# Performance work log

Hardware: AMD Instinct MI355X
Metric: run time of the kernel (lower is better)

## Reference

```python
import jax, jax.numpy as jnp
import numpy as np

B, S, D = 8, 2048, 64
NEG = -1e9


def setup_inputs() -> dict:
    key = jax.random.key(0)
    kq, kk, kv = jax.random.split(key, 3)
    return {
        "queries": jax.random.normal(kq, (B, S, D), dtype=jnp.float32),
        "keys": jax.random.normal(kk, (B, S, D), dtype=jnp.float32),
        "values": jax.random.normal(kv, (B, S, D), dtype=jnp.float32),
        "mask_q": jnp.ones((B, S), dtype=jnp.float32),
        "mask_k": jnp.ones((B, S), dtype=jnp.float32),
        "mask_v": jnp.ones((B, S), dtype=jnp.float32),
    }


def reference(queries, keys, values, mask_q, mask_k, mask_v):
    # scaled QK^T: [B, Sq, Sk]
    scaler = jnp.sqrt(jnp.asarray(queries.shape[-1], dtype=queries.dtype))
    scores = jnp.einsum("bqd,bkd->bqk", queries, keys) / scaler
    # additive padding mask from outer product of query/key masks
    padding_mask = mask_q[:, :, None] * mask_k[:, None, :]  # [B, Sq, Sk]
    scores = scores + (1.0 - padding_mask) * NEG
    attention_weights = jax.nn.softmax(scores, axis=-1)
    # mask values then weighted sum
    values = values * mask_v[:, :, None]
    output = jnp.einsum("bqk,bkd->bqd", attention_weights, values)
    return output
```

## Files before the change

### kernel.cpp

```cpp
#include <hip/hip_runtime.h>
#include <hip/hip_bf16.h>
#include <math.h>

#define BATCH 8
#define SEQ   2048
#define DIM   64
#define NEGC  (-1e9f)
#define SPLIT 4
#define TPB   8

typedef short short8  __attribute__((ext_vector_type(8)));
typedef float f32x4   __attribute__((ext_vector_type(4)));
typedef float f32x16  __attribute__((ext_vector_type(16)));

#define MFMA32(a, b, c) __builtin_amdgcn_mfma_f32_32x32x16_bf16((a), (b), (c), 0, 0, 0)

__device__ __forceinline__ ushort f2bf(float x) {
    uint u = __float_as_uint(x);
    uint r = (u + 0x7fffu + ((u >> 16) & 1u)) >> 16;
    return (ushort)r;
}
__device__ __forceinline__ float bf2f(ushort h) {
    return __uint_as_float(((uint)h) << 16);
}

__global__ __launch_bounds__(256)
void prep_kv(const float* __restrict__ K, const float* __restrict__ V,
             const float* __restrict__ MV, ushort* __restrict__ ws) {
    __shared__ float raw[64 * 68];
    const int t    = threadIdx.x;
    const int isV  = blockIdx.x >> 8;
    const int img  = blockIdx.x & 255;
    const int b    = img >> 5;
    const int tile = img & 31;
    ushort* wsI = ws + (size_t)(b * 32 + tile) * 8192;

    if (!isV) {
        const float* Kb = K + ((size_t)b * SEQ + tile * 64) * DIM;
#pragma unroll
        for (int u = 0; u < 4; u++) {
            int f = t + 256 * u, key = f >> 4, d4 = (f & 15) * 4;
            *(float4*)&raw[key * 68 + d4] = *(const float4*)(Kb + (size_t)f * 4);
        }
        __syncthreads();
#pragma unroll
        for (int u = 0; u < 2; u++) {
            int r = t + 256 * u;
            int mt = r >> 8, kc = (r >> 6) & 3, L = r & 63;
            int key = mt * 32 + (L & 31), d0 = kc * 16 + (L >> 5) * 8;
            float4 x0 = *(float4*)&raw[key * 68 + d0];
            float4 x1 = *(float4*)&raw[key * 68 + d0 + 4];
            float xs[8] = {x0.x, x0.y, x0.z, x0.w, x1.x, x1.y, x1.z, x1.w};
            short8 hv;
#pragma unroll
            for (int j = 0; j < 8; j++) hv[j] = (short)f2bf(xs[j]);
            *(short8*)(wsI + r * 8) = hv;
        }
    } else {
        const float* Vb  = V  + ((size_t)b * SEQ + tile * 64) * DIM;
        const float* MVb = MV + (size_t)b * SEQ + tile * 64;
#pragma unroll
        for (int u = 0; u < 4; u++) {
            int f = t + 256 * u, key = f >> 4, d4 = (f & 15) * 4;
            float4 x = *(const float4*)(Vb + (size_t)f * 4);
            float mv = MVb[key];
            x.x *= mv; x.y *= mv; x.z *= mv; x.w *= mv;
            *(float4*)&raw[key * 68 + d4] = x;
        }
        __syncthreads();
#pragma unroll
        for (int u = 0; u < 2; u++) {
            int r = t + 256 * u;
            int dt = r >> 8, kc = (r >> 6) & 3, L = r & 63;
            int d = dt * 32 + (L & 31), k0 = kc * 16 + (L >> 5) * 8;
            short8 ov;
#pragma unroll
            for (int j = 0; j < 8; j++) ov[j] = (short)f2bf(raw[(k0 + j) * 68 + d]);
            *(short8*)(wsI + 4096 + r * 8) = ov;
        }
    }
}

__global__ __launch_bounds__(256, 4)
void attn_main(const float* __restrict__ Q, const float* __restrict__ MQ,
               const float* __restrict__ MK, const ushort* __restrict__ ws,
               float* __restrict__ PO, float* __restrict__ ML) {
    __shared__ __align__(16) float Msc[2][64 * 36];

    const int t    = threadIdx.x;
    const int w    = t >> 6;
    const int lane = t & 63;
    const int h    = lane >> 5;
    const int lm   = lane & 31;
    const int qg   = w & 1;
    const int kh   = w >> 1;

    const int s  = blockIdx.x & 3;
    const int qb = blockIdx.x >> 2;
    const int b  = qb >> 5;
    const int qt = qb & 31;
    const int q  = qt * 64 + qg * 32 + lm;

    const float*  MKb  = MK + (size_t)b * SEQ;
    const ushort* wsKV = ws + (size_t)b * 32 * 8192;

    short8 qh[4], ql[4];
    {
        const float* Qr = Q + ((size_t)b * SEQ + q) * DIM;
#pragma unroll
        for (int kc = 0; kc < 4; kc++) {
            const float* p = Qr + kc * 16 + h * 8;
            float4 x0 = *(const float4*)p;
            float4 x1 = *(const float4*)(p + 4);
            float xs[8] = {x0.x, x0.y, x0.z, x0.w, x1.x, x1.y, x1.z, x1.w};
#pragma unroll
            for (int j = 0; j < 8; j++) {
                float v   = xs[j] * 0.125f;
                ushort hi = f2bf(v);
                ql[kc][j] = (short)f2bf(v - bf2f(hi));
                qh[kc][j] = (short)hi;
            }
        }
    }
    const float mq   = MQ[(size_t)b * SEQ + q];
    const float apen = NEGC * mq;

    float m = -1e30f, l = 0.0f;
    f32x16 ot0, ot1;
#pragma unroll
    for (int i = 0; i < 16; i++) { ot0[i] = 0.0f; ot1[i] = 0.0f; }

    short8 kf[4];
    {
        const ushort* img = wsKV + (size_t)(s * TPB) * 8192;
#pragma unroll
        for (int kc = 0; kc < 4; kc++)
            kf[kc] = *(const short8*)(img + ((kh * 4 + kc) * 64 + lane) * 8);
    }

#pragma unroll 1
    for (int tt = 0; tt < TPB; tt++) {
        const ushort* img  = wsKV + (size_t)(s * TPB + tt) * 8192;
        const ushort* imgN = (tt + 1 < TPB) ? img + 8192 : img;

        short8 kn[4];
#pragma unroll
        for (int kc = 0; kc < 4; kc++)
            kn[kc] = *(const short8*)(imgN + ((kh * 4 + kc) * 64 + lane) * 8);
        short8 vv[4];
#pragma unroll
        for (int dt = 0; dt < 2; dt++)
#pragma unroll
            for (int c = 0; c < 2; c++)
                vv[dt * 2 + c] = *(const short8*)(img + 4096 * 2 +
                                                  0);
#pragma unroll
        for (int dt = 0; dt < 2; dt++)
#pragma unroll
            for (int c = 0; c < 2; c++)
                vv[dt * 2 + c] = *(const short8*)(img + 4096 +
                    ((dt * 4 + kh * 2 + c) * 64 + lane) * 8);
        const float* mkp = MKb + (s * TPB + tt) * 64 + kh * 32 + h * 4;
        f32x4 mk0 = *(const f32x4*)(mkp + 0);
        f32x4 mk1 = *(const f32x4*)(mkp + 8);
        f32x4 mk2 = *(const f32x4*)(mkp + 16);
        f32x4 mk3 = *(const f32x4*)(mkp + 24);

        f32x16 st;
#pragma unroll
        for (int i = 0; i < 16; i++) st[i] = 0.0f;
#pragma unroll
        for (int kc = 0; kc < 4; kc++) {
            st = MFMA32(kf[kc], qh[kc], st);
            st = MFMA32(kf[kc], ql[kc], st);
        }

        float sv[16];
#pragma unroll
        for (int c = 0; c < 4; c++) {
            sv[0 * 4 + c]  = st[0 * 4 + c]  + (NEGC - apen * mk0[c]);
            sv[1 * 4 + c]  = st[1 * 4 + c]  + (NEGC - apen * mk1[c]);
            sv[2 * 4 + c]  = st[2 * 4 + c]  + (NEGC - apen * mk2[c]);
            sv[3 * 4 + c]  = st[3 * 4 + c]  + (NEGC - apen * mk3[c]);
        }
        float cm = sv[0];
#pragma unroll
        for (int i = 1; i < 16; i++) cm = fmaxf(cm, sv[i]);
        cm = fmaxf(cm, __shfl_xor(cm, 32));
        float nm    = fmaxf(m, cm);
        float alpha = __expf(m - nm);
        m = nm;

        float p[16], cs = 0.0f;
#pragma unroll
        for (int i = 0; i < 16; i++) { p[i] = __expf(sv[i] - nm); cs += p[i]; }
        cs += __shfl_xor(cs, 32);
        l   = l * alpha + cs;
        ot0 *= alpha; ot1 *= alpha;

        uint g[4][2], x[4][2];
#pragma unroll
        for (int v = 0; v < 4; v++) {
            __hip_bfloat162 c0 = __float22bfloat162_rn(make_float2(p[v*4+0], p[v*4+1]));
            __hip_bfloat162 c1 = __float22bfloat162_rn(make_float2(p[v*4+2], p[v*4+3]));
            __builtin_memcpy(&g[v][0], &c0, 4);
            __builtin_memcpy(&g[v][1], &c1, 4);
            x[v][0] = (uint)__shfl_xor((int)g[v][0], 32);
            x[v][1] = (uint)__shfl_xor((int)g[v][1], 32);
        }
        uint pbw[2][4];
        pbw[0][0] = h ? x[1][0] : g[0][0];
        pbw[0][1] = h ? x[1][1] : g[0][1];
        pbw[0][2] = h ? g[1][0] : x[0][0];
        pbw[0][3] = h ? g[1][1] : x[0][1];
        pbw[1][0] = h ? x[3][0] : g[2][0];
        pbw[1][1] = h ? x[3][1] : g[2][1];
        pbw[1][2] = h ? g[3][0] : x[2][0];
        pbw[1][3] = h ? g[3][1] : x[2][1];

#pragma unroll
        for (int c = 0; c < 2; c++) {
            short8 pb;
            __builtin_memcpy(&pb, &pbw[c][0], 16);
            ot0 = MFMA32(vv[0 * 2 + c], pb, ot0);
            ot1 = MFMA32(vv[1 * 2 + c], pb, ot1);
        }

#pragma unroll
        for (int kc = 0; kc < 4; kc++) kf[kc] = kn[kc];
    }

    if (kh == 1) {
        float* sc = &Msc[qg][lane * 36];
#pragma unroll
        for (int i = 0; i < 16; i++) { sc[i] = ot0[i]; sc[16 + i] = ot1[i]; }
        sc[32] = m;
        sc[33] = l;
    }
    __syncthreads();
    if (kh == 0) {
        const float* sc = &Msc[qg][lane * 36];
        float mb = sc[32], lb = sc[33];
        float nm = fmaxf(m, mb);
        float fa = __expf(m - nm);
        float fb = __expf(mb - nm);
        float lt = l * fa + lb * fb;

        float* po = PO + (((size_t)(s * 8 + b) * SEQ) + qt * 64 + qg * 32 + lm) * 64;
#pragma unroll
        for (int dt = 0; dt < 2; dt++) {
            const f32x16& o = dt ? ot1 : ot0;
#pragma unroll
            for (int rq = 0; rq < 4; rq++) {
                f32x4 r;
#pragma unroll
                for (int c = 0; c < 4; c++)
                    r[c] = o[rq * 4 + c] * fa + sc[dt * 16 + rq * 4 + c] * fb;
                *(f32x4*)(po + dt * 32 + rq * 8 + h * 4) = r;
            }
        }
        if (h == 0) {
            float2* ml2 = (float2*)ML;
            ml2[((size_t)(s * 8 + b) * SEQ) + qt * 64 + qg * 32 + lm] =
                make_float2(nm, lt);
        }
    }
}

__global__ __launch_bounds__(256)
void merge_o(const float* __restrict__ PO, const float* __restrict__ ML,
             float* __restrict__ O) {
    const int tid = blockIdx.x * 256 + threadIdx.x;
    const int qln = tid >> 4;
    const int dq  = tid & 15;
    const int b   = qln >> 11;
    const int qr  = qln & 2047;

    const float2* ml2 = (const float2*)ML;
    float2 mls[SPLIT];
#pragma unroll
    for (int s = 0; s < SPLIT; s++) mls[s] = ml2[(size_t)(s * 8 + b) * SEQ + qr];
    float mm = mls[0].x;
#pragma unroll
    for (int s = 1; s < SPLIT; s++) mm = fmaxf(mm, mls[s].x);
    float f[SPLIT], denom = 0.0f;
#pragma unroll
    for (int s = 0; s < SPLIT; s++) {
        f[s] = __expf(mls[s].x - mm);
        denom += mls[s].y * f[s];
    }
    float inv = 1.0f / denom;

    const size_t POS = (size_t)8 * SEQ * 64;
    const size_t o0  = ((size_t)b * SEQ + qr) * 64 + dq * 4;
    f32x4 acc = {0, 0, 0, 0};
#pragma unroll
    for (int s = 0; s < SPLIT; s++)
        acc += (*(const f32x4*)(PO + s * POS + o0)) * f[s];
    *(f32x4*)(O + ((size_t)b * SEQ + qr) * DIM + dq * 4) = acc * inv;
}

extern "C" void kernel_launch(void* const* d_in, const int* in_sizes, int n_in,
                              void* d_out, int out_size, void* d_ws, size_t ws_size,
                              hipStream_t stream) {
    const float* Q  = (const float*)d_in[0];
    const float* K  = (const float*)d_in[1];
    const float* V  = (const float*)d_in[2];
    const float* MQ = (const float*)d_in[3];
    const float* MK = (const float*)d_in[4];
    const float* MV = (const float*)d_in[5];
    float* O = (float*)d_out;

    ushort* wsKV = (ushort*)d_ws;
    float*  PO   = (float*)((char*)d_ws + (4u << 20));
    float*  ML   = (float*)((char*)d_ws + (20u << 20));

    prep_kv  <<<dim3(512),  dim3(256), 0, stream>>>(K, V, MV, wsKV);
    attn_main<<<dim3(1024), dim3(256), 0, stream>>>(Q, MQ, MK, wsKV, PO, ML);
    merge_o  <<<dim3(1024), dim3(256), 0, stream>>>(PO, ML, O);
}
```

Baseline: 107.9 us.

## Fuse KV prep, attention and merge into one cooperative grid-synced kernel

Replaces the three-kernel pipeline (KV bf16 prep, split-K attention, merge) with a single cooperative kernel. It converts K/V in a first phase, performs a grid-wide sync, then has each block own 32 queries across all 2048 keys, with four waves splitting the key chunks and combining through shared memory. This removes two launches and the partial-output/ML round trip through global memory. In exchange there is a grid barrier, lower occupancy (launch bounds 2), only 512 blocks, and each block now handles 32 queries instead of 64, so K/V reuse per block is lower.

```diff
diff --git a/kernel.cpp b/kernel.cpp
--- a/kernel.cpp
+++ b/kernel.cpp
@@ -1,13 +1,14 @@
 #include <hip/hip_runtime.h>
 #include <hip/hip_bf16.h>
+#include <hip/hip_cooperative_groups.h>
 #include <math.h>
+
+namespace cg = cooperative_groups;
 
 #define BATCH 8
 #define SEQ   2048
 #define DIM   64
 #define NEGC  (-1e9f)
-#define SPLIT 4
-#define TPB   8
 
 typedef short short8  __attribute__((ext_vector_type(8)));
 typedef float f32x4   __attribute__((ext_vector_type(4)));
@@ -24,85 +25,85 @@
     return __uint_as_float(((uint)h) << 16);
 }
 
-__global__ __launch_bounds__(256)
-void prep_kv(const float* __restrict__ K, const float* __restrict__ V,
-             const float* __restrict__ MV, ushort* __restrict__ ws) {
-    __shared__ float raw[64 * 68];
-    const int t    = threadIdx.x;
-    const int isV  = blockIdx.x >> 8;
-    const int img  = blockIdx.x & 255;
-    const int b    = img >> 5;
-    const int tile = img & 31;
-    ushort* wsI = ws + (size_t)(b * 32 + tile) * 8192;
-
-    if (!isV) {
-        const float* Kb = K + ((size_t)b * SEQ + tile * 64) * DIM;
-#pragma unroll
-        for (int u = 0; u < 4; u++) {
-            int f = t + 256 * u, key = f >> 4, d4 = (f & 15) * 4;
-            *(float4*)&raw[key * 68 + d4] = *(const float4*)(Kb + (size_t)f * 4);
-        }
-        __syncthreads();
-#pragma unroll
-        for (int u = 0; u < 2; u++) {
-            int r = t + 256 * u;
-            int mt = r >> 8, kc = (r >> 6) & 3, L = r & 63;
-            int key = mt * 32 + (L & 31), d0 = kc * 16 + (L >> 5) * 8;
-            float4 x0 = *(float4*)&raw[key * 68 + d0];
-            float4 x1 = *(float4*)&raw[key * 68 + d0 + 4];
-            float xs[8] = {x0.x, x0.y, x0.z, x0.w, x1.x, x1.y, x1.z, x1.w};
-            short8 hv;
-#pragma unroll
-            for (int j = 0; j < 8; j++) hv[j] = (short)f2bf(xs[j]);
-            *(short8*)(wsI + r * 8) = hv;
-        }
-    } else {
-        const float* Vb  = V  + ((size_t)b * SEQ + tile * 64) * DIM;
-        const float* MVb = MV + (size_t)b * SEQ + tile * 64;
-#pragma unroll
-        for (int u = 0; u < 4; u++) {
-            int f = t + 256 * u, key = f >> 4, d4 = (f & 15) * 4;
-            float4 x = *(const float4*)(Vb + (size_t)f * 4);
-            float mv = MVb[key];
-            x.x *= mv; x.y *= mv; x.z *= mv; x.w *= mv;
-            *(float4*)&raw[key * 68 + d4] = x;
-        }
-        __syncthreads();
-#pragma unroll
-        for (int u = 0; u < 2; u++) {
-            int r = t + 256 * u;
-            int dt = r >> 8, kc = (r >> 6) & 3, L = r & 63;
-            int d = dt * 32 + (L & 31), k0 = kc * 16 + (L >> 5) * 8;
-            short8 ov;
-#pragma unroll
-            for (int j = 0; j < 8; j++) ov[j] = (short)f2bf(raw[(k0 + j) * 68 + d]);
-            *(short8*)(wsI + 4096 + r * 8) = ov;
-        }
-    }
-}
-
-__global__ __launch_bounds__(256, 4)
-void attn_main(const float* __restrict__ Q, const float* __restrict__ MQ,
-               const float* __restrict__ MK, const ushort* __restrict__ ws,
-               float* __restrict__ PO, float* __restrict__ ML) {
-    __shared__ __align__(16) float Msc[2][64 * 36];
-
-    const int t    = threadIdx.x;
+__global__ __launch_bounds__(256, 2)
+void attn_all(const float* __restrict__ Q, const float* __restrict__ K,
+              const float* __restrict__ V, const float* __restrict__ MQ,
+              const float* __restrict__ MK, const float* __restrict__ MV,
+              ushort* __restrict__ ws, float* __restrict__ O) {
+    __shared__ __align__(16) float SH[6912];
+
+    const int t = threadIdx.x;
+    const int g = blockIdx.x;
+
+    {
+        const int img  = g >> 1;
+        const int isV  = g & 1;
+        const int b    = img >> 5;
+        const int tile = img & 31;
+        float* raw = SH;
+        ushort* wsI = ws + (size_t)img * 8192;
+
+        if (!isV) {
+            const float* Kb = K + ((size_t)b * SEQ + tile * 64) * DIM;
+#pragma unroll
+            for (int u = 0; u < 4; u++) {
+                int f = t + 256 * u, key = f >> 4, d4 = (f & 15) * 4;
+                *(float4*)&raw[key * 68 + d4] = *(const float4*)(Kb + (size_t)f * 4);
+            }
+            __syncthreads();
+#pragma unroll
+            for (int u = 0; u < 2; u++) {
+                int r = t + 256 * u;
+                int mt = r >> 8, kc = (r >> 6) & 3, L = r & 63;
+                int key = mt * 32 + (L & 31), d0 = kc * 16 + (L >> 5) * 8;
+                float4 x0 = *(float4*)&raw[key * 68 + d0];
+                float4 x1 = *(float4*)&raw[key * 68 + d0 + 4];
+                float xs[8] = {x0.x, x0.y, x0.z, x0.w, x1.x, x1.y, x1.z, x1.w};
+                short8 hv;
+#pragma unroll
+                for (int j = 0; j < 8; j++) hv[j] = (short)f2bf(xs[j]);
+                *(short8*)(wsI + r * 8) = hv;
+            }
+        } else {
+            const float* Vb  = V  + ((size_t)b * SEQ + tile * 64) * DIM;
+            const float* MVb = MV + (size_t)b * SEQ + tile * 64;
+#pragma unroll
+            for (int u = 0; u < 4; u++) {
+                int f = t + 256 * u, key = f >> 4, d4 = (f & 15) * 4;
+                float4 x = *(const float4*)(Vb + (size_t)f * 4);
+                float mv = MVb[key];
+                x.x *= mv; x.y *= mv; x.z *= mv; x.w *= mv;
+                *(float4*)&raw[key * 68 + d4] = x;
+            }
+            __syncthreads();
+#pragma unroll
+            for (int u = 0; u < 2; u++) {
+                int r = t + 256 * u;
+                int dt = r >> 8, kc = (r >> 6) & 3, L = r & 63;
+                int d = dt * 32 + (L & 31), k0 = kc * 16 + (L >> 5) * 8;
+                short8 ov;
+#pragma unroll
+                for (int j = 0; j < 8; j++) ov[j] = (short)f2bf(raw[(k0 + j) * 68 + d]);
+                *(short8*)(wsI + 4096 + r * 8) = ov;
+            }
+        }
+    }
+
+    __threadfence();
+    cg::this_grid().sync();
+    __threadfence();
+
     const int w    = t >> 6;
     const int lane = t & 63;
     const int h    = lane >> 5;
     const int lm   = lane & 31;
-    const int qg   = w & 1;
-    const int kh   = w >> 1;
-
-    const int s  = blockIdx.x & 3;
-    const int qb = blockIdx.x >> 2;
-    const int b  = qb >> 5;
-    const int qt = qb & 31;
-    const int q  = qt * 64 + qg * 32 + lm;
-
-    const float*  MKb  = MK + (size_t)b * SEQ;
-    const ushort* wsKV = ws + (size_t)b * 32 * 8192;
+
+    const int b  = g >> 6;
+    const int qt = g & 63;
+    const int q  = qt * 32 + lm;
+
+    const float*  MKb = MK + (size_t)b * SEQ;
+    const ushort* wsb = ws + (size_t)b * 32 * 8192;
 
     short8 qh[4], ql[4];
     {
@@ -132,35 +133,37 @@
 
     short8 kf[4];
     {
-        const ushort* img = wsKV + (size_t)(s * TPB) * 8192;
+        const int ci = w;
+        const ushort* img = wsb + (size_t)(ci >> 1) * 8192;
+        const int kh = ci & 1;
 #pragma unroll
         for (int kc = 0; kc < 4; kc++)
             kf[kc] = *(const short8*)(img + ((kh * 4 + kc) * 64 + lane) * 8);
     }
 
 #pragma unroll 1
-    for (int tt = 0; tt < TPB; tt++) {
-        const ushort* img  = wsKV + (size_t)(s * TPB + tt) * 8192;
-        const ushort* imgN = (tt + 1 < TPB) ? img + 8192 : img;
+    for (int j = 0; j < 16; j++) {
+        const int ci = j * 4 + w;
+        const int kh = ci & 1;
+        const ushort* img = wsb + (size_t)(ci >> 1) * 8192;
 
         short8 kn[4];
-#pragma unroll
-        for (int kc = 0; kc < 4; kc++)
-            kn[kc] = *(const short8*)(imgN + ((kh * 4 + kc) * 64 + lane) * 8);
+        {
+            const int cin = (j + 1 < 16) ? (j + 1) * 4 + w : ci;
+            const int khn = cin & 1;
+            const ushort* imgN = wsb + (size_t)(cin >> 1) * 8192;
+#pragma unroll
+            for (int kc = 0; kc < 4; kc++)
+                kn[kc] = *(const short8*)(imgN + ((khn * 4 + kc) * 64 + lane) * 8);
+        }
         short8 vv[4];
-#pragma unroll
-        for (int dt = 0; dt < 2; dt++)
-#pragma unroll
-            for (int c = 0; c < 2; c++)
-                vv[dt * 2 + c] = *(const short8*)(img + 4096 * 2 +
-                                                  0);
 #pragma unroll
         for (int dt = 0; dt < 2; dt++)
 #pragma unroll
             for (int c = 0; c < 2; c++)
                 vv[dt * 2 + c] = *(const short8*)(img + 4096 +
                     ((dt * 4 + kh * 2 + c) * 64 + lane) * 8);
-        const float* mkp = MKb + (s * TPB + tt) * 64 + kh * 32 + h * 4;
+        const float* mkp = MKb + ci * 32 + h * 4;
         f32x4 mk0 = *(const f32x4*)(mkp + 0);
         f32x4 mk1 = *(const f32x4*)(mkp + 8);
         f32x4 mk2 = *(const f32x4*)(mkp + 16);
@@ -178,10 +181,10 @@
         float sv[16];
 #pragma unroll
         for (int c = 0; c < 4; c++) {
-            sv[0 * 4 + c]  = st[0 * 4 + c]  + (NEGC - apen * mk0[c]);
-            sv[1 * 4 + c]  = st[1 * 4 + c]  + (NEGC - apen * mk1[c]);
-            sv[2 * 4 + c]  = st[2 * 4 + c]  + (NEGC - apen * mk2[c]);
-            sv[3 * 4 + c]  = st[3 * 4 + c]  + (NEGC - apen * mk3[c]);
+            sv[0 * 4 + c] = st[0 * 4 + c] + (NEGC - apen * mk0[c]);
+            sv[1 * 4 + c] = st[1 * 4 + c] + (NEGC - apen * mk1[c]);
+            sv[2 * 4 + c] = st[2 * 4 + c] + (NEGC - apen * mk2[c]);
+            sv[3 * 4 + c] = st[3 * 4 + c] + (NEGC - apen * mk3[c]);
         }
         float cm = sv[0];
 #pragma unroll
@@ -198,25 +201,25 @@
         l   = l * alpha + cs;
         ot0 *= alpha; ot1 *= alpha;
 
-        uint g[4][2], x[4][2];
+        uint gg[4][2], x[4][2];
 #pragma unroll
         for (int v = 0; v < 4; v++) {
             __hip_bfloat162 c0 = __float22bfloat162_rn(make_float2(p[v*4+0], p[v*4+1]));
             __hip_bfloat162 c1 = __float22bfloat162_rn(make_float2(p[v*4+2], p[v*4+3]));
-            __builtin_memcpy(&g[v][0], &c0, 4);
-            __builtin_memcpy(&g[v][1], &c1, 4);
-            x[v][0] = (uint)__shfl_xor((int)g[v][0], 32);
-            x[v][1] = (uint)__shfl_xor((int)g[v][1], 32);
+            __builtin_memcpy(&gg[v][0], &c0, 4);
+            __builtin_memcpy(&gg[v][1], &c1, 4);
+            x[v][0] = (uint)__shfl_xor((int)gg[v][0], 32);
+            x[v][1] = (uint)__shfl_xor((int)gg[v][1], 32);
         }
         uint pbw[2][4];
-        pbw[0][0] = h ? x[1][0] : g[0][0];
-        pbw[0][1] = h ? x[1][1] : g[0][1];
-        pbw[0][2] = h ? g[1][0] : x[0][0];
-        pbw[0][3] = h ? g[1][1] : x[0][1];
-        pbw[1][0] = h ? x[3][0] : g[2][0];
-        pbw[1][1] = h ? x[3][1] : g[2][1];
-        pbw[1][2] = h ? g[3][0] : x[2][0];
-        pbw[1][3] = h ? g[3][1] : x[2][1];
+        pbw[0][0] = h ? x[1][0] : gg[0][0];
+        pbw[0][1] = h ? x[1][1] : gg[0][1];
+        pbw[0][2] = h ? gg[1][0] : x[0][0];
+        pbw[0][3] = h ? gg[1][1] : x[0][1];
+        pbw[1][0] = h ? x[3][0] : gg[2][0];
+        pbw[1][1] = h ? x[3][1] : gg[2][1];
+        pbw[1][2] = h ? gg[3][0] : x[2][0];
+        pbw[1][3] = h ? gg[3][1] : x[2][1];
 
 #pragma unroll
         for (int c = 0; c < 2; c++) {
@@ -230,23 +233,46 @@
         for (int kc = 0; kc < 4; kc++) kf[kc] = kn[kc];
     }
 
-    if (kh == 1) {
-        float* sc = &Msc[qg][lane * 36];
+    __syncthreads();
+    if (w > 0) {
+        float* sc = SH + ((size_t)(w - 1) * 64 + lane) * 36;
 #pragma unroll
         for (int i = 0; i < 16; i++) { sc[i] = ot0[i]; sc[16 + i] = ot1[i]; }
         sc[32] = m;
         sc[33] = l;
     }
     __syncthreads();
-    if (kh == 0) {
-        const float* sc = &Msc[qg][lane * 36];
-        float mb = sc[32], lb = sc[33];
-        float nm = fmaxf(m, mb);
-        float fa = __expf(m - nm);
-        float fb = __expf(mb - nm);
-        float lt = l * fa + lb * fb;
-
-        float* po = PO + (((size_t)(s * 8 + b) * SEQ) + qt * 64 + qg * 32 + lm) * 64;
+    if (w == 0) {
+        float mw[3], lw[3];
+        float M = m;
+#pragma unroll
+        for (int wv = 0; wv < 3; wv++) {
+            const float* sc = SH + ((size_t)wv * 64 + lane) * 36;
+            mw[wv] = sc[32];
+            lw[wv] = sc[33];
+            M = fmaxf(M, mw[wv]);
+        }
+        float fa = __expf(m - M);
+        float lt = l * fa;
+        ot0 *= fa; ot1 *= fa;
+#pragma unroll
+        for (int wv = 0; wv < 3; wv++) {
+            const float* sc = SH + ((size_t)wv * 64 + lane) * 36;
+            float f = __expf(mw[wv] - M);
+            lt += lw[wv] * f;
+#pragma unroll
+            for (int i = 0; i < 4; i++) {
+                f32x4 a0 = *(const f32x4*)&sc[i * 4];
+                f32x4 a1 = *(const f32x4*)&sc[16 + i * 4];
+#pragma unroll
+                for (int c = 0; c < 4; c++) {
+                    ot0[i * 4 + c] += a0[c] * f;
+                    ot1[i * 4 + c] += a1[c] * f;
+                }
+            }
+        }
+        float inv = 1.0f / lt;
+        float* Orow = O + ((size_t)b * SEQ + q) * DIM;
 #pragma unroll
         for (int dt = 0; dt < 2; dt++) {
             const f32x16& o = dt ? ot1 : ot0;
@@ -254,50 +280,11 @@
             for (int rq = 0; rq < 4; rq++) {
                 f32x4 r;
 #pragma unroll
-                for (int c = 0; c < 4; c++)
-                    r[c] = o[rq * 4 + c] * fa + sc[dt * 16 + rq * 4 + c] * fb;
-                *(f32x4*)(po + dt * 32 + rq * 8 + h * 4) = r;
-            }
-        }
-        if (h == 0) {
-            float2* ml2 = (float2*)ML;
-            ml2[((size_t)(s * 8 + b) * SEQ) + qt * 64 + qg * 32 + lm] =
-                make_float2(nm, lt);
-        }
-    }
-}
-
-__global__ __launch_bounds__(256)
-void merge_o(const float* __restrict__ PO, const float* __restrict__ ML,
-             float* __restrict__ O) {
-    const int tid = blockIdx.x * 256 + threadIdx.x;
-    const int qln = tid >> 4;
-    const int dq  = tid & 15;
-    const int b   = qln >> 11;
-    const int qr  = qln & 2047;
-
-    const float2* ml2 = (const float2*)ML;
-    float2 mls[SPLIT];
-#pragma unroll
-    for (int s = 0; s < SPLIT; s++) mls[s] = ml2[(size_t)(s * 8 + b) * SEQ + qr];
-    float mm = mls[0].x;
-#pragma unroll
-    for (int s = 1; s < SPLIT; s++) mm = fmaxf(mm, mls[s].x);
-    float f[SPLIT], denom = 0.0f;
-#pragma unroll
-    for (int s = 0; s < SPLIT; s++) {
-        f[s] = __expf(mls[s].x - mm);
-        denom += mls[s].y * f[s];
-    }
-    float inv = 1.0f / denom;
-
-    const size_t POS = (size_t)8 * SEQ * 64;
-    const size_t o0  = ((size_t)b * SEQ + qr) * 64 + dq * 4;
-    f32x4 acc = {0, 0, 0, 0};
-#pragma unroll
-    for (int s = 0; s < SPLIT; s++)
-        acc += (*(const f32x4*)(PO + s * POS + o0)) * f[s];
-    *(f32x4*)(O + ((size_t)b * SEQ + qr) * DIM + dq * 4) = acc * inv;
+                for (int c = 0; c < 4; c++) r[c] = o[rq * 4 + c] * inv;
+                *(f32x4*)(Orow + dt * 32 + rq * 8 + h * 4) = r;
+            }
+        }
+    }
 }
 
 extern "C" void kernel_launch(void* const* d_in, const int* in_sizes, int n_in,
@@ -309,13 +296,11 @@
     const float* MQ = (const float*)d_in[3];
     const float* MK = (const float*)d_in[4];
     const float* MV = (const float*)d_in[5];
-    float* O = (float*)d_out;
-
-    ushort* wsKV = (ushort*)d_ws;
-    float*  PO   = (float*)((char*)d_ws + (4u << 20));
-    float*  ML   = (float*)((char*)d_ws + (20u << 20));
-
-    prep_kv  <<<dim3(512),  dim3(256), 0, stream>>>(K, V, MV, wsKV);
-    attn_main<<<dim3(1024), dim3(256), 0, stream>>>(Q, MQ, MK, wsKV, PO, ML);
-    merge_o  <<<dim3(1024), dim3(256), 0, stream>>>(PO, ML, O);
+    float* O   = (float*)d_out;
+    ushort* ws = (ushort*)d_ws;
+
+    void* args[] = {(void*)&Q, (void*)&K, (void*)&V, (void*)&MQ,
+                    (void*)&MK, (void*)&MV, (void*)&ws, (void*)&O};
+    hipLaunchCooperativeKernel((const void*)attn_all, dim3(512), dim3(256),
+                               args, 0, stream);
 }
```

After: 283.8 us. 2.63x slower.
